# Kernel tuning notes

Hardware: AMD Instinct MI355X
Metric: run time of the kernel (lower is better)

The kernel has to match this reference:

```python
import jax, jax.numpy as jnp
import numpy as np
import math

HEAD_DIM = 128
THETA = 10000.0
MASK_VAL = -10000.0


def _rope(x, cos, sin):
    # x: (B, S, D); cos/sin: (S, D//2). Pairs (even, odd) rotated as complex.
    xr = x.reshape(*x.shape[:-1], -1, 2)
    xe, xo = xr[..., 0], xr[..., 1]
    oe = xe * cos - xo * sin
    oo = xe * sin + xo * cos
    return jnp.stack([oe, oo], axis=-1).reshape(x.shape)


def setup_inputs() -> dict:
    key = jax.random.key(0)
    B, S, D = 8, 4096, HEAD_DIM
    qkv = jax.random.normal(key, (B, S, 3 * D), dtype=jnp.float32)
    return {"qkv": qkv}


def reference(qkv):
    B, S, threeD = qkv.shape
    D = threeD // 3
    qkv = qkv.reshape(B, S, 3, D)
    q, k, v = qkv[:, :, 0], qkv[:, :, 1], qkv[:, :, 2]

    # precompute_freqs_cis: outer(t, 1/theta^(2i/d)) -> cos/sin (S, D//2)
    inv_freq = 1.0 / (THETA ** (jnp.arange(0, D, 2, dtype=jnp.float32) / D))
    freqs = jnp.arange(S, dtype=jnp.float32)[:, None] * inv_freq[None, :]
    cos, sin = jnp.cos(freqs), jnp.sin(freqs)
    q = _rope(q, cos, sin)
    k = _rope(k, cos, sin)

    scale = 1.0 / math.sqrt(D)
    scores = jnp.einsum('btd,bsd->bts', q, k) * scale  # (B, S, S)
    causal_mask = jnp.triu(jnp.full((S, S), MASK_VAL, dtype=scores.dtype), 1)
    attn = jax.nn.softmax(scores + causal_mask, axis=-1)
    out = jnp.einsum('bts,bsd->btd', attn, v)  # (B, S, D)
    return out
```

## Files before the change

### kernel.cpp

```cpp
#include <hip/hip_runtime.h>
#include <math.h>

typedef _Float16 half8 __attribute__((ext_vector_type(8)));
typedef float floatx4 __attribute__((ext_vector_type(4)));
typedef float floatx2 __attribute__((ext_vector_type(2)));

#define B_ 8
#define S_ 4096
#define SCALE_L2E 0.12751743008389106f
#define MASK_L2E  -14426.950408889634f
#define L2_10K_OVER_128 0.10381025296522975f

#define PLD 72
#define KW  136
#define VW  24
#define OSTLD 136
#define SLOTS_PER_B 576

__device__ __forceinline__ int chunk_prefix(int qt32) {
    int g = qt32 >> 4;
    return qt32 + 8 * g * (g - 1) + (qt32 - (g << 4)) * g;
}

__global__ __launch_bounds__(256) void prep_kernel(const float* __restrict__ qkv,
                                                   _Float16* __restrict__ Qh,
                                                   _Float16* __restrict__ Kp,
                                                   _Float16* __restrict__ Vp) {
    __shared__ __align__(16) _Float16 Kl[16][KW];
    __shared__ __align__(16) _Float16 Vt[128][VW];
    const int tid = threadIdx.x;
    const int b   = blockIdx.y;
    const int s0  = blockIdx.x * 16;

#pragma unroll
    for (int it = 0; it < 4; ++it) {
        int idx = tid + it * 256;
        int i = idx & 63, sr = idx >> 6, s = s0 + sr;
        const float* base = qkv + ((size_t)(b * S_ + s)) * 384 + 2 * i;
        floatx2 q2 = *(const floatx2*)base;
        floatx2 k2 = *(const floatx2*)(base + 128);
        float inv = exp2f(-(float)(2 * i) * L2_10K_OVER_128);
        float ang = (float)s * inv;
        float sn, cs;
        __sincosf(ang, &sn, &cs);
        size_t oq = ((size_t)(b * S_ + s)) * 128 + 2 * i;
        Qh[oq]     = (_Float16)((q2[0] * cs - q2[1] * sn) * SCALE_L2E);
        Qh[oq + 1] = (_Float16)((q2[0] * sn + q2[1] * cs) * SCALE_L2E);
        Kl[sr][2 * i]     = (_Float16)(k2[0] * cs - k2[1] * sn);
        Kl[sr][2 * i + 1] = (_Float16)(k2[0] * sn + k2[1] * cs);
    }
#pragma unroll
    for (int it = 0; it < 2; ++it) {
        int idx = tid + it * 256;
        int c = idx & 31, sr = idx >> 5;
        floatx4 v = *(const floatx4*)(qkv + ((size_t)(b * S_ + s0 + sr)) * 384 + 256 + c * 4);
#pragma unroll
        for (int j = 0; j < 4; ++j) Vt[c * 4 + j][sr] = (_Float16)v[j];
    }
    __syncthreads();

    {
        int c = tid >> 6, lane = tid & 63;
        int quad = lane >> 4, n = lane & 15;
        half8 val = *(const half8*)&Kl[n][c * 32 + quad * 8];
        int s16 = s0 >> 4;
        *(half8*)(Kp + (((size_t)(b * 256 + s16) * 4 + c) * 64 + lane) * 8) = val;
    }
    {
        int kt = s0 >> 6, c2 = (s0 >> 5) & 1, qp = (s0 >> 4) & 1;
        int nt = tid >> 5, lq = (tid >> 4) & 1, n = tid & 15;
        int quad = qp * 2 + lq;
        int lane = quad * 16 + n;
        half8 val = *(const half8*)&Vt[nt * 16 + n][lq * 8];
        *(half8*)(Vp + ((((size_t)(b * 64 + kt) * 2 + c2) * 8 + nt) * 64 + lane) * 8) = val;
    }
}

__global__ __launch_bounds__(256) void attn_part_kernel(const _Float16* __restrict__ Qh,
                                                        const _Float16* __restrict__ Kp,
                                                        const _Float16* __restrict__ Vp,
                                                        _Float16* __restrict__ Ppart,
                                                        float* __restrict__ Lpart) {
    __shared__ __align__(16) _Float16 SH[4 * 4 * 16 * PLD];

    const int tid   = threadIdx.x;
    const int w     = tid >> 6;
    const int lane  = tid & 63;
    const int quad  = lane >> 4;
    const int l16   = lane & 15;
    const int b     = blockIdx.x & 7;
    const int chunk = blockIdx.x >> 3;
    const int qt32  = 127 - (blockIdx.y * 4 + w);
    const int qr0   = qt32 * 32;
    const int kt_max = (qr0 + 31) >> 6;
    const int c0    = chunk * 8;
    if (c0 > kt_max) return;
    const int kend  = min(kt_max, c0 + 7);
    const int slot  = b * SLOTS_PER_B + chunk_prefix(qt32) + chunk;
    _Float16* SHw = SH + w * (4 * 16 * PLD);

    half8 aq[2][4];
#pragma unroll
    for (int tile = 0; tile < 2; ++tile) {
        const _Float16* Qb = Qh + ((size_t)(b * S_) + qr0 + tile * 16 + l16) * 128;
#pragma unroll
        for (int c = 0; c < 4; ++c) aq[tile][c] = *(const half8*)(Qb + c * 32 + quad * 8);
    }

    floatx4 o[2][8];
#pragma unroll
    for (int tile = 0; tile < 2; ++tile)
#pragma unroll
        for (int i = 0; i < 8; ++i) o[tile][i] = (floatx4){0.f, 0.f, 0.f, 0.f};
    float rsum[2][4] = {{0.f, 0.f, 0.f, 0.f}, {0.f, 0.f, 0.f, 0.f}};

    const _Float16* Kb = Kp + (size_t)b * 524288;
    const _Float16* Vb = Vp + (size_t)b * 524288;

    for (int kt = c0; kt <= kend; ++kt) {
        floatx4 s4[2][4];
#pragma unroll
        for (int t = 0; t < 4; ++t) {
            const _Float16* kp = Kb + (((size_t)(kt * 16 + t * 4)) * 64 + lane) * 8;
            half8 bk[4];
#pragma unroll
            for (int c = 0; c < 4; ++c) bk[c] = *(const half8*)(kp + c * 512);
            floatx4 a0 = (floatx4){0.f, 0.f, 0.f, 0.f};
            floatx4 a1 = (floatx4){0.f, 0.f, 0.f, 0.f};
            __builtin_amdgcn_s_setprio(1);
#pragma unroll
            for (int c = 0; c < 4; ++c) {
                a0 = __builtin_amdgcn_mfma_f32_16x16x32_f16(aq[0][c], bk[c], a0, 0, 0, 0);
                a1 = __builtin_amdgcn_mfma_f32_16x16x32_f16(aq[1][c], bk[c], a1, 0, 0, 0);
            }
            __builtin_amdgcn_s_setprio(0);
            s4[0][t] = a0; s4[1][t] = a1;
        }

        if (kt == kt_max) {
#pragma unroll
            for (int tile = 0; tile < 2; ++tile)
#pragma unroll
                for (int t = 0; t < 4; ++t)
#pragma unroll
                    for (int r = 0; r < 4; ++r) {
                        int kcol = kt * 64 + t * 16 + l16;
                        int qr   = qr0 + tile * 16 + quad * 4 + r;
                        if (kcol > qr) s4[tile][t][r] += MASK_L2E;
                    }
        }

        const int buf = kt & 1;
#pragma unroll
        for (int tile = 0; tile < 2; ++tile)
#pragma unroll
            for (int t = 0; t < 4; ++t)
#pragma unroll
                for (int r = 0; r < 4; ++r) {
                    float p = __builtin_amdgcn_exp2f(s4[tile][t][r]);
                    rsum[tile][r] += p;
                    SHw[(tile * 2 + buf) * (16 * PLD) + (quad * 4 + r) * PLD + t * 16 + l16] = (_Float16)p;
                }

#pragma unroll
        for (int c2 = 0; c2 < 2; ++c2) {
            half8 vf[8];
#pragma unroll
            for (int nt = 0; nt < 8; ++nt)
                vf[nt] = *(const half8*)(Vb + (((size_t)(kt * 2 + c2) * 8 + nt) * 64 + lane) * 8);
#pragma unroll
            for (int tile = 0; tile < 2; ++tile) {
                half8 ap = *(const half8*)&SHw[(tile * 2 + buf) * (16 * PLD) + l16 * PLD + c2 * 32 + quad * 8];
                __builtin_amdgcn_s_setprio(1);
#pragma unroll
                for (int nt = 0; nt < 8; ++nt)
                    o[tile][nt] = __builtin_amdgcn_mfma_f32_16x16x32_f16(ap, vf[nt], o[tile][nt], 0, 0, 0);
                __builtin_amdgcn_s_setprio(0);
            }
        }
    }

#pragma unroll
    for (int off = 1; off <= 8; off <<= 1)
#pragma unroll
        for (int tile = 0; tile < 2; ++tile)
#pragma unroll
            for (int r = 0; r < 4; ++r)
                rsum[tile][r] += __shfl_xor(rsum[tile][r], off, 64);
    if (l16 == 0) {
#pragma unroll
        for (int tile = 0; tile < 2; ++tile)
#pragma unroll
            for (int r = 0; r < 4; ++r)
                Lpart[(size_t)slot * 32 + tile * 16 + quad * 4 + r] = rsum[tile][r];
    }

    _Float16* Ost = SHw;
#pragma unroll
    for (int tile = 0; tile < 2; ++tile)
#pragma unroll
        for (int nt = 0; nt < 8; ++nt)
#pragma unroll
            for (int r = 0; r < 4; ++r)
                Ost[(tile * 16 + quad * 4 + r) * OSTLD + nt * 16 + l16] = (_Float16)o[tile][nt][r];
    _Float16* pp = Ppart + (size_t)slot * 4096;
#pragma unroll
    for (int i = 0; i < 8; ++i) {
        int idx = lane + i * 64;
        half8 v = *(const half8*)&Ost[(idx >> 4) * OSTLD + (idx & 15) * 8];
        *(half8*)(pp + (size_t)idx * 8) = v;
    }
}

__global__ __launch_bounds__(256) void reduce_kernel(const _Float16* __restrict__ Ppart,
                                                     const float* __restrict__ Lpart,
                                                     float* __restrict__ out) {
    const int bid  = blockIdx.x;
    const int b    = bid >> 7;
    const int qt32 = bid & 127;
    const int qr0  = qt32 * 32;
    const int nch  = (((qr0 + 31) >> 6) >> 3) + 1;
    const int slot0 = b * SLOTS_PER_B + chunk_prefix(qt32);
    const _Float16* pp = Ppart + (size_t)slot0 * 4096;
    const float* lp = Lpart + (size_t)slot0 * 32;
    const int tid = threadIdx.x;

#pragma unroll
    for (int j = 0; j < 2; ++j) {
        int idx = tid + j * 256;
        int row = idx >> 4;
        float acc[8] = {0.f, 0.f, 0.f, 0.f, 0.f, 0.f, 0.f, 0.f};
        float l = 0.f;
        for (int c = 0; c < nch; ++c) {
            half8 v = *(const half8*)(pp + (size_t)c * 4096 + (size_t)idx * 8);
#pragma unroll
            for (int k = 0; k < 8; ++k) acc[k] += (float)v[k];
            l += lp[c * 32 + row];
        }
        float inv = 1.0f / l;
        float* ob = out + ((size_t)(b * S_) + qr0) * 128 + (size_t)idx * 8;
        floatx4 o0 = (floatx4){acc[0] * inv, acc[1] * inv, acc[2] * inv, acc[3] * inv};
        floatx4 o1 = (floatx4){acc[4] * inv, acc[5] * inv, acc[6] * inv, acc[7] * inv};
        *(floatx4*)ob = o0;
        *(floatx4*)(ob + 4) = o1;
    }
}

__global__ __launch_bounds__(64) void attn_atomic_kernel(const _Float16* __restrict__ Qh,
                                                         const _Float16* __restrict__ Kp,
                                                         const _Float16* __restrict__ Vp,
                                                         float* __restrict__ out,
                                                         float* __restrict__ Lg) {
    __shared__ __align__(16) _Float16 Pl[2][16 * PLD];
    const int lane = threadIdx.x, quad = lane >> 4, l16 = lane & 15;
    const int b = blockIdx.x & 7, chunk = blockIdx.x >> 3;
    const int qt = 255 - blockIdx.y, qr0 = qt * 16;
    const int kt_max = qt >> 2, c0 = chunk * 8;
    if (c0 > kt_max) return;
    const int kend = min(kt_max, c0 + 7);
    const _Float16* Qb = Qh + ((size_t)(b * S_) + qr0 + l16) * 128;
    half8 aq[4];
#pragma unroll
    for (int c = 0; c < 4; ++c) aq[c] = *(const half8*)(Qb + c * 32 + quad * 8);
    floatx4 o[8];
#pragma unroll
    for (int i = 0; i < 8; ++i) o[i] = (floatx4){0.f, 0.f, 0.f, 0.f};
    float rsum[4] = {0.f, 0.f, 0.f, 0.f};
    const _Float16* Kb = Kp + (size_t)b * 524288;
    const _Float16* Vb = Vp + (size_t)b * 524288;
    for (int kt = c0; kt <= kend; ++kt) {
        half8 vf[2][8];
#pragma unroll
        for (int c2 = 0; c2 < 2; ++c2)
#pragma unroll
            for (int nt = 0; nt < 8; ++nt)
                vf[c2][nt] = *(const half8*)(Vb + (((size_t)(kt * 2 + c2) * 8 + nt) * 64 + lane) * 8);
        floatx4 s4[4];
#pragma unroll
        for (int t = 0; t < 4; ++t) {
            const _Float16* kp = Kb + ((size_t)((kt * 4 + t) * 4) * 64 + lane) * 8;
            floatx4 acc = (floatx4){0.f, 0.f, 0.f, 0.f};
#pragma unroll
            for (int c = 0; c < 4; ++c) {
                half8 bk = *(const half8*)(kp + c * 512);
                acc = __builtin_amdgcn_mfma_f32_16x16x32_f16(aq[c], bk, acc, 0, 0, 0);
            }
            s4[t] = acc;
        }
        if (kt == kt_max) {
#pragma unroll
            for (int t = 0; t < 4; ++t)
#pragma unroll
                for (int r = 0; r < 4; ++r) {
                    int kcol = kt * 64 + t * 16 + l16;
                    int qr = qr0 + quad * 4 + r;
                    if (kcol > qr) s4[t][r] += MASK_L2E;
                }
        }
        const int buf = kt & 1;
#pragma unroll
        for (int t = 0; t < 4; ++t)
#pragma unroll
            for (int r = 0; r < 4; ++r) {
                float p = __builtin_amdgcn_exp2f(s4[t][r]);
                rsum[r] += p;
                Pl[buf][(quad * 4 + r) * PLD + t * 16 + l16] = (_Float16)p;
            }
#pragma unroll
        for (int c2 = 0; c2 < 2; ++c2) {
            half8 ap = *(const half8*)&Pl[buf][l16 * PLD + c2 * 32 + quad * 8];
#pragma unroll
            for (int nt = 0; nt < 8; ++nt)
                o[nt] = __builtin_amdgcn_mfma_f32_16x16x32_f16(ap, vf[c2][nt], o[nt], 0, 0, 0);
        }
    }
#pragma unroll
    for (int off = 1; off <= 8; off <<= 1)
#pragma unroll
        for (int r = 0; r < 4; ++r)
            rsum[r] += __shfl_xor(rsum[r], off, 64);
    if (l16 == 0) {
#pragma unroll
        for (int r = 0; r < 4; ++r)
            atomicAdd(&Lg[(size_t)(b * S_) + qr0 + quad * 4 + r], rsum[r]);
    }
    float* ob = out + ((size_t)(b * S_) + qr0) * 128;
#pragma unroll
    for (int nt = 0; nt < 8; ++nt)
#pragma unroll
        for (int r = 0; r < 4; ++r)
            atomicAdd(&ob[(quad * 4 + r) * 128 + nt * 16 + l16], o[nt][r]);
}

__global__ __launch_bounds__(256) void norm_kernel(float* __restrict__ out,
                                                   const float* __restrict__ Lg) {
    int i = blockIdx.x * 256 + threadIdx.x;
    int row = i >> 5;
    floatx4 v = *(floatx4*)(out + (size_t)i * 4);
    float inv = 1.0f / Lg[row];
    v[0] *= inv; v[1] *= inv; v[2] *= inv; v[3] *= inv;
    *(floatx4*)(out + (size_t)i * 4) = v;
}

extern "C" void kernel_launch(void* const* d_in, const int* in_sizes, int n_in,
                              void* d_out, int out_size, void* d_ws, size_t ws_size,
                              hipStream_t stream) {
    const float* qkv = (const float*)d_in[0];
    float* out = (float*)d_out;
    const size_t MB = 1024 * 1024;
    _Float16* Qh = (_Float16*)d_ws;
    _Float16* Kp = (_Float16*)((char*)d_ws + 8 * MB);
    _Float16* Vp = (_Float16*)((char*)d_ws + 16 * MB);

    const size_t lpart_bytes = (size_t)B_ * SLOTS_PER_B * 32 * sizeof(float);
    const size_t ppart_bytes = (size_t)B_ * SLOTS_PER_B * 4096 * sizeof(_Float16);
    const size_t need = 25 * MB + ppart_bytes;

    prep_kernel<<<dim3(256, B_), dim3(256), 0, stream>>>(qkv, Qh, Kp, Vp);

    if (ws_size >= need) {
        float*    Lpart = (float*)((char*)d_ws + 24 * MB);
        _Float16* Ppart = (_Float16*)((char*)d_ws + 25 * MB);
        (void)lpart_bytes;
        attn_part_kernel<<<dim3(64, 32), dim3(256), 0, stream>>>(Qh, Kp, Vp, Ppart, Lpart);
        reduce_kernel<<<dim3(1024), dim3(256), 0, stream>>>(Ppart, Lpart, out);
    } else {
        float* Lg = (float*)((char*)d_ws + 24 * MB);
        hipMemsetAsync(out, 0, (size_t)B_ * S_ * 128 * sizeof(float), stream);
        hipMemsetAsync(Lg, 0, (size_t)B_ * S_ * sizeof(float), stream);
        attn_atomic_kernel<<<dim3(64, 256), dim3(64), 0, stream>>>(Qh, Kp, Vp, out, Lg);
        norm_kernel<<<dim3(4096), dim3(256), 0, stream>>>(out, Lg);
    }
}
```

Before: 167.7 us.

## Stage K/V tiles in LDS via async global_load_lds, shared across 8 waves

Block size goes from 4 to 8 waves, and each block covers 8 query tiles of 32 rows instead of 4. Per-key-tile K and V fragments (16KB each) are loaded once per block into double-buffered LDS with global_load_lds and shared by all waves. The next tile is prefetched while the current one is computed, with barriers between steps. This cuts redundant global/L2 traffic for K/V, at the cost of barrier synchronization, idle waves on causal-boundary tiles, and higher LDS use that lowers occupancy.

```diff
diff --git a/kernel.cpp b/kernel.cpp
--- a/kernel.cpp
+++ b/kernel.cpp
@@ -16,10 +16,17 @@
 #define VW  24
 #define OSTLD 136
 #define SLOTS_PER_B 576
+#define NW 8
+#define KVTILE 8192
 
 __device__ __forceinline__ int chunk_prefix(int qt32) {
     int g = qt32 >> 4;
     return qt32 + 8 * g * (g - 1) + (qt32 - (g << 4)) * g;
+}
+
+__device__ __forceinline__ void glds16(const _Float16* src, _Float16* dst) {
+    __builtin_amdgcn_global_load_lds((const __attribute__((address_space(1))) void*)src,
+                                     (__attribute__((address_space(3))) void*)dst, 16, 0, 0);
 }
 
 __global__ __launch_bounds__(256) void prep_kernel(const float* __restrict__ qkv,
@@ -76,28 +83,35 @@
     }
 }
 
-__global__ __launch_bounds__(256) void attn_part_kernel(const _Float16* __restrict__ Qh,
+__global__ __launch_bounds__(512) void attn_part_kernel(const _Float16* __restrict__ Qh,
                                                         const _Float16* __restrict__ Kp,
                                                         const _Float16* __restrict__ Vp,
                                                         _Float16* __restrict__ Ppart,
                                                         float* __restrict__ Lpart) {
-    __shared__ __align__(16) _Float16 SH[4 * 4 * 16 * PLD];
-
-    const int tid   = threadIdx.x;
-    const int w     = tid >> 6;
-    const int lane  = tid & 63;
-    const int quad  = lane >> 4;
-    const int l16   = lane & 15;
+    __shared__ __align__(16) _Float16 KVs[2][2][KVTILE];
+    __shared__ __align__(16) _Float16 Psh[NW][4 * 16 * PLD];
+
+    const int tid  = threadIdx.x;
+    const int w    = tid >> 6;
+    const int lane = tid & 63;
+    const int quad = lane >> 4;
+    const int l16  = lane & 15;
     const int b     = blockIdx.x & 7;
     const int chunk = blockIdx.x >> 3;
-    const int qt32  = 127 - (blockIdx.y * 4 + w);
-    const int qr0   = qt32 * 32;
+    const int c0    = chunk * 8;
+
+    const int qt32_top  = 127 - blockIdx.y * 8;
+    const int ktmax_blk = (qt32_top * 32 + 31) >> 6;
+    if (c0 > ktmax_blk) return;
+    const int kend_blk  = min(ktmax_blk, c0 + 7);
+
+    const int qt32   = qt32_top - w;
+    const int qr0    = qt32 * 32;
     const int kt_max = (qr0 + 31) >> 6;
-    const int c0    = chunk * 8;
-    if (c0 > kt_max) return;
-    const int kend  = min(kt_max, c0 + 7);
-    const int slot  = b * SLOTS_PER_B + chunk_prefix(qt32) + chunk;
-    _Float16* SHw = SH + w * (4 * 16 * PLD);
+    const bool has_work = (c0 <= kt_max);
+    const int kend   = min(kt_max, c0 + 7);
+    const int slot   = b * SLOTS_PER_B + chunk_prefix(qt32) + chunk;
+    _Float16* SHw = &Psh[w][0];
 
     half8 aq[2][4];
 #pragma unroll
@@ -117,68 +131,99 @@
     const _Float16* Kb = Kp + (size_t)b * 524288;
     const _Float16* Vb = Vp + (size_t)b * 524288;
 
-    for (int kt = c0; kt <= kend; ++kt) {
-        floatx4 s4[2][4];
-#pragma unroll
-        for (int t = 0; t < 4; ++t) {
-            const _Float16* kp = Kb + (((size_t)(kt * 16 + t * 4)) * 64 + lane) * 8;
-            half8 bk[4];
-#pragma unroll
-            for (int c = 0; c < 4; ++c) bk[c] = *(const half8*)(kp + c * 512);
-            floatx4 a0 = (floatx4){0.f, 0.f, 0.f, 0.f};
-            floatx4 a1 = (floatx4){0.f, 0.f, 0.f, 0.f};
-            __builtin_amdgcn_s_setprio(1);
-#pragma unroll
-            for (int c = 0; c < 4; ++c) {
-                a0 = __builtin_amdgcn_mfma_f32_16x16x32_f16(aq[0][c], bk[c], a0, 0, 0, 0);
-                a1 = __builtin_amdgcn_mfma_f32_16x16x32_f16(aq[1][c], bk[c], a1, 0, 0, 0);
+    {
+        const _Float16* ks = Kb + (size_t)c0 * KVTILE + (w * 2) * 512 + lane * 8;
+        const _Float16* vs = Vb + (size_t)c0 * KVTILE + (w * 2) * 512 + lane * 8;
+        _Float16* kd = &KVs[c0 & 1][0][(w * 2) * 512];
+        _Float16* vd = &KVs[c0 & 1][1][(w * 2) * 512];
+        glds16(ks, kd);       glds16(vs, vd);
+        glds16(ks + 512, kd + 512); glds16(vs + 512, vd + 512);
+    }
+
+    for (int kt = c0; kt <= kend_blk; ++kt) {
+        const int buf = kt & 1;
+        if (kt < kend_blk) {
+            const _Float16* ks = Kb + (size_t)(kt + 1) * KVTILE + (w * 2) * 512 + lane * 8;
+            const _Float16* vs = Vb + (size_t)(kt + 1) * KVTILE + (w * 2) * 512 + lane * 8;
+            _Float16* kd = &KVs[buf ^ 1][0][(w * 2) * 512];
+            _Float16* vd = &KVs[buf ^ 1][1][(w * 2) * 512];
+            glds16(ks, kd);       glds16(vs, vd);
+            glds16(ks + 512, kd + 512); glds16(vs + 512, vd + 512);
+            asm volatile("s_waitcnt vmcnt(4)" ::: "memory");
+        } else {
+            asm volatile("s_waitcnt vmcnt(0)" ::: "memory");
+        }
+        __builtin_amdgcn_s_barrier();
+
+        if (has_work && kt <= kend) {
+            const _Float16* Klds = &KVs[buf][0][0];
+            const _Float16* Vlds = &KVs[buf][1][0];
+
+            floatx4 s4[2][4];
+#pragma unroll
+            for (int t = 0; t < 4; ++t) {
+                half8 bk[4];
+#pragma unroll
+                for (int c = 0; c < 4; ++c)
+                    bk[c] = *(const half8*)&Klds[((t * 4 + c) * 64 + lane) * 8];
+                floatx4 a0 = (floatx4){0.f, 0.f, 0.f, 0.f};
+                floatx4 a1 = (floatx4){0.f, 0.f, 0.f, 0.f};
+                __builtin_amdgcn_s_setprio(1);
+#pragma unroll
+                for (int c = 0; c < 4; ++c) {
+                    a0 = __builtin_amdgcn_mfma_f32_16x16x32_f16(aq[0][c], bk[c], a0, 0, 0, 0);
+                    a1 = __builtin_amdgcn_mfma_f32_16x16x32_f16(aq[1][c], bk[c], a1, 0, 0, 0);
+                }
+                __builtin_amdgcn_s_setprio(0);
+                s4[0][t] = a0; s4[1][t] = a1;
             }
-            __builtin_amdgcn_s_setprio(0);
-            s4[0][t] = a0; s4[1][t] = a1;
-        }
-
-        if (kt == kt_max) {
+
+            if (kt == kt_max) {
+#pragma unroll
+                for (int tile = 0; tile < 2; ++tile)
+#pragma unroll
+                    for (int t = 0; t < 4; ++t)
+#pragma unroll
+                        for (int r = 0; r < 4; ++r) {
+                            int kcol = kt * 64 + t * 16 + l16;
+                            int qr   = qr0 + tile * 16 + quad * 4 + r;
+                            if (kcol > qr) s4[tile][t][r] += MASK_L2E;
+                        }
+            }
+
 #pragma unroll
             for (int tile = 0; tile < 2; ++tile)
 #pragma unroll
                 for (int t = 0; t < 4; ++t)
 #pragma unroll
                     for (int r = 0; r < 4; ++r) {
-                        int kcol = kt * 64 + t * 16 + l16;
-                        int qr   = qr0 + tile * 16 + quad * 4 + r;
-                        if (kcol > qr) s4[tile][t][r] += MASK_L2E;
+                        float p = __builtin_amdgcn_exp2f(s4[tile][t][r]);
+                        rsum[tile][r] += p;
+                        SHw[(tile * 2 + buf) * (16 * PLD) + (quad * 4 + r) * PLD + t * 16 + l16] = (_Float16)p;
                     }
-        }
-
-        const int buf = kt & 1;
-#pragma unroll
-        for (int tile = 0; tile < 2; ++tile)
-#pragma unroll
-            for (int t = 0; t < 4; ++t)
-#pragma unroll
-                for (int r = 0; r < 4; ++r) {
-                    float p = __builtin_amdgcn_exp2f(s4[tile][t][r]);
-                    rsum[tile][r] += p;
-                    SHw[(tile * 2 + buf) * (16 * PLD) + (quad * 4 + r) * PLD + t * 16 + l16] = (_Float16)p;
+
+#pragma unroll
+            for (int c2 = 0; c2 < 2; ++c2) {
+                half8 vf[8];
+#pragma unroll
+                for (int nt = 0; nt < 8; ++nt)
+                    vf[nt] = *(const half8*)&Vlds[((c2 * 8 + nt) * 64 + lane) * 8];
+#pragma unroll
+                for (int tile = 0; tile < 2; ++tile) {
+                    half8 ap = *(const half8*)&SHw[(tile * 2 + buf) * (16 * PLD) + l16 * PLD + c2 * 32 + quad * 8];
+                    __builtin_amdgcn_s_setprio(1);
+#pragma unroll
+                    for (int nt = 0; nt < 8; ++nt)
+                        o[tile][nt] = __builtin_amdgcn_mfma_f32_16x16x32_f16(ap, vf[nt], o[tile][nt], 0, 0, 0);
+                    __builtin_amdgcn_s_setprio(0);
                 }
-
-#pragma unroll
-        for (int c2 = 0; c2 < 2; ++c2) {
-            half8 vf[8];
-#pragma unroll
-            for (int nt = 0; nt < 8; ++nt)
-                vf[nt] = *(const half8*)(Vb + (((size_t)(kt * 2 + c2) * 8 + nt) * 64 + lane) * 8);
-#pragma unroll
-            for (int tile = 0; tile < 2; ++tile) {
-                half8 ap = *(const half8*)&SHw[(tile * 2 + buf) * (16 * PLD) + l16 * PLD + c2 * 32 + quad * 8];
-                __builtin_amdgcn_s_setprio(1);
-#pragma unroll
-                for (int nt = 0; nt < 8; ++nt)
-                    o[tile][nt] = __builtin_amdgcn_mfma_f32_16x16x32_f16(ap, vf[nt], o[tile][nt], 0, 0, 0);
-                __builtin_amdgcn_s_setprio(0);
             }
         }
-    }
+        asm volatile("" ::: "memory");
+        __builtin_amdgcn_s_barrier();
+    }
+
+    if (!has_work) return;
 
 #pragma unroll
     for (int off = 1; off <= 8; off <<= 1)
@@ -362,7 +407,7 @@
         float*    Lpart = (float*)((char*)d_ws + 24 * MB);
         _Float16* Ppart = (_Float16*)((char*)d_ws + 25 * MB);
         (void)lpart_bytes;
-        attn_part_kernel<<<dim3(64, 32), dim3(256), 0, stream>>>(Qh, Kp, Vp, Ppart, Lpart);
+        attn_part_kernel<<<dim3(64, 16), dim3(512), 0, stream>>>(Qh, Kp, Vp, Ppart, Lpart);
         reduce_kernel<<<dim3(1024), dim3(256), 0, stream>>>(Ppart, Lpart, out);
     } else {
         float* Lg = (float*)((char*)d_ws + 24 * MB);
```

Result: no change. 165.0 us (-1.6%).
